# Optimization experiments

Measured on AMD Instinct MI355X. Metric: run time of the kernel, lower is better.

Reference implementation:

```python
import jax, jax.numpy as jnp
import numpy as np

B, HI, WI, CV, CT, T = 8, 64, 64, 512, 512, 77
HH, DH = 8, 64
TOP_M, TOPP, CLAMP_LOGIT, TAU, ALPHA0 = 5, 0.9, 2.0, 0.5, 0.1


def setup_inputs() -> dict:
    key = jax.random.key(0)
    ks = jax.random.split(key, 12)
    s = 0.02
    w = lambda k, shp: jax.random.normal(k, shp, jnp.float32) * s
    return {
        "visual": jax.random.normal(ks[0], (B, HI, WI, CV), jnp.float32),
        "text": jax.random.normal(ks[1], (B, T, CT), jnp.float32),
        "ln1_g": jnp.ones((CV,), jnp.float32), "ln1_b": jnp.zeros((CV,), jnp.float32),
        "ln2_g": jnp.ones((CV,), jnp.float32), "ln2_b": jnp.zeros((CV,), jnp.float32),
        "Wq": w(ks[2], (CV, CV)), "bq": jnp.zeros((CV,), jnp.float32),
        "Wk": w(ks[3], (CT, CV)), "bk": jnp.zeros((CV,), jnp.float32),
        "Wv": w(ks[4], (CT, CV)), "bv": jnp.zeros((CV,), jnp.float32),
        "Wo": w(ks[5], (CV, CV)), "bo": jnp.zeros((CV,), jnp.float32),
        "Wg": w(ks[6], (CV, 1)), "bg": jnp.zeros((1,), jnp.float32),
        "W1": w(ks[7], (CV, 4 * CV)), "b1": jnp.zeros((4 * CV,), jnp.float32),
        "W2": w(ks[8], (4 * CV, CV)), "b2": jnp.zeros((CV,), jnp.float32),
        "logit_scale": jnp.asarray(np.log(1.0 / 0.07), jnp.float32),
        "alpha": jnp.asarray(ALPHA0, jnp.float32),
    }


def _ln(x, g, b, eps=1e-5):
    m = x.mean(-1, keepdims=True)
    v = ((x - m) ** 2).mean(-1, keepdims=True)
    return (x - m) * jax.lax.rsqrt(v + eps) * g + b


def _l2norm(t, eps=1e-6):  # F.normalize: x / max(||x||, eps)
    return t / jnp.maximum(jnp.linalg.norm(t, axis=-1, keepdims=True), eps)


def _sam_forward(visual, text, ln1_g, ln1_b, ln2_g, ln2_b, Wq, bq, Wk, bk, Wv, bv,
                 Wo, bo, Wg, bg, W1, b1, W2, b2, logit_scale, alpha):
    Bx, Hi, Wi, C = visual.shape
    N = Hi * Wi
    x = _ln(visual, ln1_g, ln1_b).reshape(Bx, N, C)          # pre-LN, [B,N,Cv]
    q_full = x @ Wq + bq
    k_full = text @ Wk + bk
    v_full = text @ Wv + bv
    pad = jnp.abs(text).sum(-1) <= 1e-6                      # [B,T] all-zero tokens
    q = _l2norm(q_full).reshape(Bx, N, HH, DH)               # normalize over full Cv, then split heads
    k = _l2norm(k_full).reshape(Bx, -1, HH, DH)
    v = v_full.reshape(Bx, -1, HH, DH)
    scale = jnp.exp(jnp.clip(logit_scale, -CLAMP_LOGIT, CLAMP_LOGIT)) / jnp.sqrt(jnp.float32(DH))
    sim = jnp.einsum("bnhd,bthd->bnht", q, k) * scale        # [B,N,H,T]
    sim = jnp.where(pad[:, None, None, :], -jnp.inf, sim)
    # top-m sparsify (keep entries >= kth largest)
    if TOP_M < sim.shape[-1]:
        kth = jax.lax.top_k(sim, TOP_M)[0][..., -1:]
        sim = jnp.where(sim >= kth, sim, -jnp.inf)
    attn = jax.nn.softmax(sim, axis=-1)
    # top-p nucleus: sort desc, keep cum<=p (always keep top-1), scatter back, renorm
    idx = jnp.argsort(-attn, axis=-1)
    prob = jnp.take_along_axis(attn, idx, axis=-1)
    keep = (jnp.cumsum(prob, axis=-1) <= TOPP).astype(attn.dtype)
    keep = keep.at[..., 0].set(1.0)
    inv = jnp.argsort(idx, axis=-1)
    sparse = jnp.take_along_axis(keep * prob, inv, axis=-1)
    attn = sparse / jnp.maximum(sparse.sum(-1, keepdims=True), 1e-6)
    # entropy-based confidence, [B,N,1]
    ah = attn.transpose(0, 2, 1, 3)                          # [B,H,N,T]
    maxp = ah.max(-1, keepdims=True)
    t_eff = jnp.maximum((ah > 0).astype(attn.dtype).sum(-1, keepdims=True), 1.0)
    denom = jnp.log(jnp.maximum(t_eff, 2.0))
    pc = jnp.maximum(ah, 1e-8)
    entropy = -(pc * jnp.log(pc)).sum(-1, keepdims=True) / denom
    conf = jnp.clip(maxp * (1.0 - entropy), 0.0, 1.0).mean(axis=1)
    aligned = jnp.einsum("bnht,bthd->bnhd", attn, v).reshape(Bx, N, C)
    aligned = aligned @ Wo + bo
    # trust region: cap ||aligned|| at tau * rms(x)
    x_rms = jnp.sqrt((x ** 2).mean(-1, keepdims=True)) + 1e-6
    a_norm = jnp.sqrt((aligned ** 2).sum(-1, keepdims=True))
    aligned = aligned * jnp.minimum(TAU * x_rms / jnp.maximum(a_norm, 1e-6), 1.0)
    gate = jax.nn.sigmoid(x @ Wg + bg) * conf
    y = x + alpha * gate * aligned
    h = jax.nn.gelu(_ln(y, ln2_g, ln2_b) @ W1 + b1, approximate=False)
    y = y + (h @ W2 + b2)
    return y.reshape(Bx, Hi, Wi, C)


def reference(visual, text, ln1_g, ln1_b, ln2_g, ln2_b, Wq, bq, Wk, bk, Wv, bv,
              Wo, bo, Wg, bg, W1, b1, W2, b2, logit_scale, alpha):
    return _sam_forward(visual, text, ln1_g, ln1_b, ln2_g, ln2_b, Wq, bq, Wk, bk,
                        Wv, bv, Wo, bo, Wg, bg, W1, b1, W2, b2, logit_scale, alpha)
```

## Files before the change

### kernel.cpp

```cpp
#include <hip/hip_runtime.h>
#include <hip/hip_bf16.h>
#include <math.h>

#define NROW 32768
#define CVC  512
#define T77  77
#define BT   616
#define HHC  8
#define DHC  64

typedef __attribute__((ext_vector_type(8))) short bf16x8;
typedef __attribute__((ext_vector_type(4))) float f32x4;

__device__ __forceinline__ void gload_lds16(const void* g, void* l) {
  __builtin_amdgcn_global_load_lds(
      (__attribute__((address_space(1))) void*)g,
      (__attribute__((address_space(3))) void*)l, 16, 0, 0);
}

__device__ __forceinline__ float wave_reduce_sum(float v) {
  #pragma unroll
  for (int s = 32; s > 0; s >>= 1) v += __shfl_xor(v, s, 64);
  return v;
}

__global__ __launch_bounds__(256)
void stats1_kernel(const float* __restrict__ visual, const float* __restrict__ g,
                   const float* __restrict__ b, const float* __restrict__ Wg,
                   const float* __restrict__ bg,
                   float* __restrict__ mean1, float* __restrict__ rstd1,
                   float* __restrict__ xrms, float* __restrict__ gpre,
                   __hip_bfloat16* __restrict__ xbf) {
  const int lane = threadIdx.x & 63;
  const int row  = blockIdx.x * 4 + (threadIdx.x >> 6);
  const float* vr = visual + (size_t)row * CVC + lane * 8;
  float4 va = *(const float4*)vr;
  float4 vb = *(const float4*)(vr + 4);
  float v[8] = {va.x, va.y, va.z, va.w, vb.x, vb.y, vb.z, vb.w};
  float s = 0.f;
  #pragma unroll
  for (int i = 0; i < 8; i++) s += v[i];
  float m = wave_reduce_sum(s) * (1.0f / CVC);
  float s2 = 0.f;
  #pragma unroll
  for (int i = 0; i < 8; i++) { float d = v[i] - m; s2 += d * d; }
  float rs = rsqrtf(wave_reduce_sum(s2) * (1.0f / CVC) + 1e-5f);
  const float4 g0 = *(const float4*)(g + lane * 8), g1v = *(const float4*)(g + lane * 8 + 4);
  const float4 b0 = *(const float4*)(b + lane * 8), b1v = *(const float4*)(b + lane * 8 + 4);
  const float4 w0 = *(const float4*)(Wg + lane * 8), w1 = *(const float4*)(Wg + lane * 8 + 4);
  float gg[8] = {g0.x, g0.y, g0.z, g0.w, g1v.x, g1v.y, g1v.z, g1v.w};
  float bb[8] = {b0.x, b0.y, b0.z, b0.w, b1v.x, b1v.y, b1v.z, b1v.w};
  float ww[8] = {w0.x, w0.y, w0.z, w0.w, w1.x, w1.y, w1.z, w1.w};
  float x[8], sx2 = 0.f, sg = 0.f;
  union { bf16x8 v8; __hip_bfloat16 h[8]; } u;
  #pragma unroll
  for (int i = 0; i < 8; i++) {
    x[i] = (v[i] - m) * rs * gg[i] + bb[i];
    sx2 += x[i] * x[i];
    sg  += x[i] * ww[i];
    u.h[i] = __float2bfloat16(x[i]);
  }
  *(bf16x8*)(xbf + (size_t)row * CVC + lane * 8) = u.v8;
  sx2 = wave_reduce_sum(sx2);
  sg  = wave_reduce_sum(sg);
  if (lane == 0) {
    mean1[row] = m; rstd1[row] = rs;
    xrms[row] = sqrtf(sx2 * (1.0f / CVC)) + 1e-6f;
    gpre[row] = sg + bg[0];
  }
}

__global__ void convT_kernel(const float* __restrict__ W, __hip_bfloat16* __restrict__ Wt,
                             int K, int N) {
  __shared__ float t[32][33];
  int n0 = blockIdx.x * 32, k0 = blockIdx.y * 32;
  int tx = threadIdx.x, ty = threadIdx.y;
  #pragma unroll
  for (int i = 0; i < 32; i += 8) t[ty + i][tx] = W[(size_t)(k0 + ty + i) * N + n0 + tx];
  __syncthreads();
  #pragma unroll
  for (int i = 0; i < 32; i += 8)
    Wt[(size_t)(n0 + ty + i) * K + k0 + tx] = __float2bfloat16(t[tx][ty + i]);
}

template<int EPI>
__global__ __launch_bounds__(512, 2)
void mfma_gemm(const __hip_bfloat16* __restrict__ A, const __hip_bfloat16* __restrict__ Bt,
               const float* __restrict__ bias, float* __restrict__ out,
               __hip_bfloat16* __restrict__ outbf, float* __restrict__ ps,
               int M, int N, int K) {
  __shared__ __align__(16) char lds[131072];
  const int tid = threadIdx.x;
  const int lane = tid & 63;
  const int wid  = tid >> 6;

  const int nwg  = gridDim.x * gridDim.y;
  const int orig = blockIdx.y * gridDim.x + blockIdx.x;
  const int wg   = (orig & 7) * (nwg >> 3) + (orig >> 3);
  const int bx = wg % gridDim.x;
  const int by = wg / gridDim.x;
  const int bm = by * 256, bn = bx * 256;

  const int wm = wid >> 2, wn = wid & 3;
  const int lrow = lane & 15, kq = lane >> 4;

  f32x4 acc[8][4] = {};

  const int r_in = lane >> 3;
  const int cblk = (lane & 7) ^ r_in;
  const __hip_bfloat16* gA = A  + (size_t)(bm + r_in) * K + cblk * 8;
  const __hip_bfloat16* gB = Bt + (size_t)(bn + r_in) * K + cblk * 8;
  char* ldsA = lds;
  char* ldsB = lds + 65536;

  auto stageA = [&](int buf, int k0, int half) {
    #pragma unroll
    for (int j = 0; j < 2; j++) {
      int R0 = half * 128 + wid * 16 + j * 8;
      gload_lds16(gA + (size_t)R0 * K + k0, ldsA + buf * 32768 + R0 * 128);
    }
  };
  auto stageB = [&](int buf, int k0, int half) {
    #pragma unroll
    for (int j = 0; j < 2; j++) {
      int R0 = half * 128 + wid * 16 + j * 8;
      gload_lds16(gB + (size_t)R0 * K + k0, ldsB + buf * 32768 + R0 * 128);
    }
  };

  const int swz = lrow & 7;
  auto ldA = [&](int buf, int m, int kk) -> bf16x8 {
    int r = wm * 128 + m * 16 + lrow;
    int blk = (kk * 4 + kq) ^ swz;
    return *(const bf16x8*)(ldsA + buf * 32768 + r * 128 + blk * 16);
  };
  auto ldB = [&](int buf, int n, int kk) -> bf16x8 {
    int r = wn * 64 + n * 16 + lrow;
    int blk = (kk * 4 + kq) ^ swz;
    return *(const bf16x8*)(ldsB + buf * 32768 + r * 128 + blk * 16);
  };

  const int NT = K >> 6;
  stageB(0, 0, 0); stageB(0, 0, 1);
  stageA(0, 0, 0); stageA(0, 0, 1);
  stageB(1, 64, 0); stageB(1, 64, 1);

  bf16x8 af[4][2], bfv[4][2];
  for (int t = 0; t < NT; ++t) {
    const int cur = t & 1;
    if (t < NT - 1) {
      asm volatile("s_waitcnt vmcnt(4)" ::: "memory");
    } else {
      asm volatile("s_waitcnt vmcnt(0)" ::: "memory");
    }
    __builtin_amdgcn_s_barrier();
    asm volatile("" ::: "memory");

    #pragma unroll
    for (int m = 0; m < 4; m++) { af[m][0] = ldA(cur, m, 0); af[m][1] = ldA(cur, m, 1); }
    #pragma unroll
    for (int n = 0; n < 2; n++) { bfv[n][0] = ldB(cur, n, 0); bfv[n][1] = ldB(cur, n, 1); }
    if (t + 1 < NT) stageA(cur ^ 1, (t + 1) << 6, 0);
    __builtin_amdgcn_s_setprio(1);
    #pragma unroll
    for (int m = 0; m < 4; m++)
      #pragma unroll
      for (int n = 0; n < 2; n++) {
        acc[m][n] = __builtin_amdgcn_mfma_f32_16x16x32_bf16(af[m][0], bfv[n][0], acc[m][n], 0, 0, 0);
        acc[m][n] = __builtin_amdgcn_mfma_f32_16x16x32_bf16(af[m][1], bfv[n][1], acc[m][n], 0, 0, 0);
      }
    __builtin_amdgcn_s_setprio(0);

    #pragma unroll
    for (int n = 2; n < 4; n++) { bfv[n][0] = ldB(cur, n, 0); bfv[n][1] = ldB(cur, n, 1); }
    if (t + 1 < NT) stageA(cur ^ 1, (t + 1) << 6, 1);
    __builtin_amdgcn_s_setprio(1);
    #pragma unroll
    for (int m = 0; m < 4; m++)
      #pragma unroll
      for (int n = 2; n < 4; n++) {
        acc[m][n] = __builtin_amdgcn_mfma_f32_16x16x32_bf16(af[m][0], bfv[n][0], acc[m][n], 0, 0, 0);
        acc[m][n] = __builtin_amdgcn_mfma_f32_16x16x32_bf16(af[m][1], bfv[n][1], acc[m][n], 0, 0, 0);
      }
    __builtin_amdgcn_s_setprio(0);

    asm volatile("s_waitcnt lgkmcnt(0)" ::: "memory");
    __builtin_amdgcn_s_barrier();
    asm volatile("" ::: "memory");

    #pragma unroll
    for (int m = 0; m < 4; m++) { af[m][0] = ldA(cur, m + 4, 0); af[m][1] = ldA(cur, m + 4, 1); }
    if (t + 2 < NT) stageB(cur, (t + 2) << 6, 0);
    __builtin_amdgcn_s_setprio(1);
    #pragma unroll
    for (int m = 0; m < 4; m++)
      #pragma unroll
      for (int n = 0; n < 2; n++) {
        acc[m + 4][n] = __builtin_amdgcn_mfma_f32_16x16x32_bf16(af[m][0], bfv[n][0], acc[m + 4][n], 0, 0, 0);
        acc[m + 4][n] = __builtin_amdgcn_mfma_f32_16x16x32_bf16(af[m][1], bfv[n][1], acc[m + 4][n], 0, 0, 0);
      }
    __builtin_amdgcn_s_setprio(0);

    if (t + 2 < NT) stageB(cur, (t + 2) << 6, 1);
    __builtin_amdgcn_s_setprio(1);
    #pragma unroll
    for (int m = 0; m < 4; m++)
      #pragma unroll
      for (int n = 2; n < 4; n++) {
        acc[m + 4][n] = __builtin_amdgcn_mfma_f32_16x16x32_bf16(af[m][0], bfv[n][0], acc[m + 4][n], 0, 0, 0);
        acc[m + 4][n] = __builtin_amdgcn_mfma_f32_16x16x32_bf16(af[m][1], bfv[n][1], acc[m + 4][n], 0, 0, 0);
      }
    __builtin_amdgcn_s_setprio(0);
  }

  const int c0 = bn + wn * 64 + lrow;
  if (EPI == 1) {
    __syncthreads();
    char* eb = lds + wid * 16384;
    #pragma unroll
    for (int n = 0; n < 4; n++) {
      float bval = bias[c0 + n * 16];
      #pragma unroll
      for (int m = 0; m < 8; m++) {
        #pragma unroll
        for (int rg = 0; rg < 4; rg++) {
          int lr  = m * 16 + kq * 4 + rg;
          int lcb = (n * 32 + lrow * 2) ^ (kq << 5);
          float v = acc[m][n][rg] + bval;
          float ge = v / (1.0f + __expf(v * (-1.5957691216f - 0.0713548162f * v * v)));
          *(__hip_bfloat16*)(eb + lr * 128 + lcb) = __float2bfloat16(ge);
        }
      }
    }
    asm volatile("s_waitcnt lgkmcnt(0)" ::: "memory");
    __builtin_amdgcn_sched_barrier(0);
    const int rr = lane >> 3, bb = lane & 7;
    #pragma unroll
    for (int it = 0; it < 16; it++) {
      int lr  = it * 8 + rr;
      int lcb = (bb << 4) ^ (((lr >> 2) & 3) << 5);
      uint4 v = *(const uint4*)(eb + lr * 128 + lcb);
      size_t go = (size_t)(bm + wm * 128 + lr) * N + (bn + wn * 64 + bb * 8);
      *(uint4*)(&outbf[go]) = v;
    }
  } else if (EPI == 3) {
    __syncthreads();
    char* eb = lds + wid * 16384;
    float bv4[4];
    #pragma unroll
    for (int n = 0; n < 4; n++) bv4[n] = bias[c0 + n * 16];
    const int psi = (bn >> 8) * 4 + wn;
    #pragma unroll
    for (int m = 0; m < 8; m++) {
      #pragma unroll
      for (int rg = 0; rg < 4; rg++) {
        int lr = m * 16 + kq * 4 + rg;
        float ss = 0.f;
        #pragma unroll
        for (int n = 0; n < 4; n++) {
          float v = acc[m][n][rg] + bv4[n];
          ss += v * v;
          int lcb = (n * 32 + lrow * 2) ^ (kq << 5);
          *(__hip_bfloat16*)(eb + lr * 128 + lcb) = __float2bfloat16(v);
        }
        ss += __shfl_xor(ss, 1, 64); ss += __shfl_xor(ss, 2, 64);
        ss += __shfl_xor(ss, 4, 64); ss += __shfl_xor(ss, 8, 64);
        if (lrow == 0) ps[(size_t)psi * M + (bm + wm * 128 + lr)] = ss;
      }
    }
    asm volatile("s_waitcnt lgkmcnt(0)" ::: "memory");
    __builtin_amdgcn_sched_barrier(0);
    const int rr = lane >> 3, bb = lane & 7;
    #pragma unroll
    for (int it = 0; it < 16; it++) {
      int lr  = it * 8 + rr;
      int lcb = (bb << 4) ^ (((lr >> 2) & 3) << 5);
      uint4 v = *(const uint4*)(eb + lr * 128 + lcb);
      size_t go = (size_t)(bm + wm * 128 + lr) * N + (bn + wn * 64 + bb * 8);
      *(uint4*)(&outbf[go]) = v;
    }
  } else {
    __syncthreads();
    char* eb = lds + wid * 16384;
    const int rr = lane >> 4, bb = lane & 15;
    #pragma unroll
    for (int half = 0; half < 2; half++) {
      if (half) {
        asm volatile("s_waitcnt lgkmcnt(0)" ::: "memory");
        __builtin_amdgcn_sched_barrier(0);
      }
      #pragma unroll
      for (int n = 0; n < 4; n++) {
        float bval = bias[c0 + n * 16];
        #pragma unroll
        for (int m = 0; m < 4; m++) {
          #pragma unroll
          for (int rg = 0; rg < 4; rg++) {
            int lr  = m * 16 + kq * 4 + rg;
            int byo = (n * 64 + lrow * 4) ^ (kq << 6);
            *(float*)(eb + lr * 256 + byo) = acc[half * 4 + m][n][rg] + bval;
          }
        }
      }
      asm volatile("s_waitcnt lgkmcnt(0)" ::: "memory");
      __builtin_amdgcn_sched_barrier(0);
      #pragma unroll
      for (int it = 0; it < 16; it++) {
        int lr  = it * 4 + rr;
        int byo = (bb * 16) ^ (((lr >> 2) & 3) << 6);
        float4 v4 = *(const float4*)(eb + lr * 256 + byo);
        size_t go = (size_t)(bm + wm * 128 + half * 64 + lr) * N + (bn + wn * 64 + bb * 4);
        if (EPI == 0) {
          *(float4*)(&out[go]) = v4;
        } else {
          const float4 o = *(const float4*)(&out[go]);
          v4.x += o.x; v4.y += o.y; v4.z += o.z; v4.w += o.w;
          *(float4*)(&out[go]) = v4;
        }
      }
    }
  }
}

__global__ void kv2_gemm(const float* __restrict__ A,
                         const float* __restrict__ Wk, const float* __restrict__ bk,
                         const float* __restrict__ Wv, const float* __restrict__ bv,
                         float* __restrict__ KF, float* __restrict__ VF,
                         int M, int K, int N) {
  __shared__ float As[16][68];
  __shared__ float Bs[16][68];
  const bool isV = blockIdx.y >= 10;
  const float* W    = isV ? Wv : Wk;
  const float* bias = isV ? bv : bk;
  float* out        = isV ? VF : KF;
  int tid = threadIdx.x;
  int bm = (isV ? blockIdx.y - 10 : blockIdx.y) * 64, bn = blockIdx.x * 64;
  int ty = tid >> 4, tx = tid & 15;
  float acc[4][4] = {};
  for (int k0 = 0; k0 < K; k0 += 16) {
    #pragma unroll
    for (int i = 0; i < 4; i++) {
      int idx = tid + i * 256;
      int mm = idx >> 4, kk = idx & 15;
      int row = bm + mm;
      As[kk][mm] = (row < M) ? A[(size_t)row * K + k0 + kk] : 0.f;
    }
    #pragma unroll
    for (int i = 0; i < 4; i++) {
      int idx = tid + i * 256;
      int kk = idx >> 6, nn = idx & 63;
      Bs[kk][nn] = W[(size_t)(k0 + kk) * N + bn + nn];
    }
    __syncthreads();
    #pragma unroll
    for (int kk = 0; kk < 16; kk++) {
      float4 av = *(const float4*)&As[kk][ty * 4];
      float4 bv4 = *(const float4*)&Bs[kk][tx * 4];
      float a_[4] = {av.x, av.y, av.z, av.w};
      float b_[4] = {bv4.x, bv4.y, bv4.z, bv4.w};
      #pragma unroll
      for (int i = 0; i < 4; i++)
        #pragma unroll
        for (int j = 0; j < 4; j++)
          acc[i][j] = fmaf(a_[i], b_[j], acc[i][j]);
    }
    __syncthreads();
  }
  #pragma unroll
  for (int i = 0; i < 4; i++) {
    int row = bm + ty * 4 + i;
    if (row >= M) continue;
    #pragma unroll
    for (int j = 0; j < 4; j++) {
      int col = bn + tx * 4 + j;
      out[(size_t)row * N + col] = acc[i][j] + bias[col];
    }
  }
}

__global__ __launch_bounds__(256)
void l2norm_kernel(const __hip_bfloat16* __restrict__ qf, const float* __restrict__ ps,
                   __hip_bfloat16* __restrict__ qbf) {
  const int lane = threadIdx.x & 63;
  const int row  = blockIdx.x * 4 + (threadIdx.x >> 6);
  float s = 0.f;
  #pragma unroll
  for (int j = 0; j < 8; j++) s += ps[(size_t)j * NROW + row];
  float inv = 1.0f / fmaxf(sqrtf(s), 1e-6f);
  union { bf16x8 v8; __hip_bfloat16 h[8]; } u;
  u.v8 = *(const bf16x8*)(qf + (size_t)row * CVC + lane * 8);
  #pragma unroll
  for (int i = 0; i < 8; i++)
    u.h[i] = __float2bfloat16(__bfloat162float(u.h[i]) * inv);
  *(bf16x8*)(qbf + (size_t)row * CVC + lane * 8) = u.v8;
}

__global__ __launch_bounds__(256)
void knorm_kernel(float* __restrict__ kf, const float* __restrict__ text,
                  int* __restrict__ pad) {
  const int lane = threadIdx.x & 63;
  const int row  = blockIdx.x * 4 + (threadIdx.x >> 6);
  float* p = kf + (size_t)row * CVC + lane * 8;
  const float* tx = text + (size_t)row * CVC + lane * 8;
  float4 va = *(const float4*)p;
  float4 vb = *(const float4*)(p + 4);
  float4 ta = *(const float4*)tx;
  float4 tb = *(const float4*)(tx + 4);
  float v[8] = {va.x, va.y, va.z, va.w, vb.x, vb.y, vb.z, vb.w};
  float t[8] = {ta.x, ta.y, ta.z, ta.w, tb.x, tb.y, tb.z, tb.w};
  float s = 0.f, a = 0.f;
  #pragma unroll
  for (int i = 0; i < 8; i++) { s += v[i] * v[i]; a += fabsf(t[i]); }
  s = wave_reduce_sum(s);
  a = wave_reduce_sum(a);
  float inv = 1.0f / fmaxf(sqrtf(s), 1e-6f);
  float4 o0 = {v[0] * inv, v[1] * inv, v[2] * inv, v[3] * inv};
  float4 o1 = {v[4] * inv, v[5] * inv, v[6] * inv, v[7] * inv};
  *(float4*)p = o0;
  *(float4*)(p + 4) = o1;
  if (lane == 0) pad[row] = (a <= 1e-6f) ? 1 : 0;
}

__global__ void kbf_kernel(const float* __restrict__ kf, __hip_bfloat16* __restrict__ kbf) {
  int bh = blockIdx.x;
  int b = bh >> 3, h = bh & 7;
  int tid = threadIdx.x;
  for (int i = tid; i < 80 * 64; i += 256) {
    int t = i >> 6, d = i & 63;
    float v = (t < T77) ? kf[(size_t)(b * T77 + t) * CVC + h * DHC + d] : 0.0f;
    kbf[(size_t)bh * (80 * 64) + i] = __float2bfloat16(v);
  }
}

__global__ __launch_bounds__(256)
void simA_kernel(const __hip_bfloat16* __restrict__ qbf, const __hip_bfloat16* __restrict__ kbf,
                 float* __restrict__ sim) {
  const int tid = threadIdx.x;
  const int wid = tid >> 6, lane = tid & 63;
  const int r0 = blockIdx.x * 64 + wid * 16;
  const int b = (blockIdx.x * 64) >> 12;
  const int lrow = lane & 15, kq = lane >> 4;
  const __hip_bfloat16* qrow = qbf + (size_t)(r0 + lrow) * CVC;
  for (int h = 0; h < HHC; h++) {
    const __hip_bfloat16* kb = kbf + (size_t)(b * 8 + h) * (80 * 64);
    f32x4 acc[5] = {};
    #pragma unroll
    for (int ks = 0; ks < 2; ks++) {
      bf16x8 af = *(const bf16x8*)(qrow + h * DHC + ks * 32 + kq * 8);
      #pragma unroll
      for (int n = 0; n < 5; n++) {
        bf16x8 bf = *(const bf16x8*)(kb + (size_t)(n * 16 + lrow) * DHC + ks * 32 + kq * 8);
        acc[n] = __builtin_amdgcn_mfma_f32_16x16x32_bf16(af, bf, acc[n], 0, 0, 0);
      }
    }
    #pragma unroll
    for (int n = 0; n < 5; n++)
      #pragma unroll
      for (int rg = 0; rg < 4; rg++)
        sim[(size_t)(r0 + kq * 4 + rg) * 640 + h * 80 + n * 16 + lrow] = acc[n][rg];
  }
}

__global__ __launch_bounds__(256)
void attnB_kernel(const float* __restrict__ sim, const float* __restrict__ vf,
                  const int* __restrict__ pad, const float* __restrict__ ls,
                  float* __restrict__ conf_out, __hip_bfloat16* __restrict__ abf) {
  __shared__ float spr[32][HHC][5];
  __shared__ int   sti[32][HHC][5];
  __shared__ float sconf[256];
  __shared__ float sbias[80];
  const int tid = threadIdx.x;
  const int r = tid >> 3, h = tid & 7;
  const int r0 = blockIdx.x * 32;
  const int b = r0 >> 12;
  const float lsv = fminf(fmaxf(ls[0], -2.0f), 2.0f);
  const float scale = expf(lsv) * 0.125f;

  if (tid < 80) sbias[tid] = (tid < T77 && !pad[b * T77 + tid]) ? 0.0f : -INFINITY;
  __syncthreads();

  float t0 = -INFINITY, t1 = -INFINITY, t2 = -INFINITY, t3 = -INFINITY, t4 = -INFINITY;
  int   i0 = -1, i1 = -1, i2 = -1, i3 = -1, i4 = -1;
  const float4* simp = (const float4*)(sim + (size_t)(r0 + r) * 640 + h * 80);
  #pragma unroll
  for (int tt = 0; tt < 20; tt++) {
    float4 v4 = simp[tt];
    #pragma unroll
    for (int j = 0; j < 4; j++) {
      int t = tt * 4 + j;
      float sv = (j == 0 ? v4.x : j == 1 ? v4.y : j == 2 ? v4.z : v4.w);
      float s = sv * scale + sbias[t];
      if (s > t4) {
        t4 = s; i4 = t;
        if (t4 > t3) { float f = t3; t3 = t4; t4 = f; int x = i3; i3 = i4; i4 = x; }
        if (t3 > t2) { float f = t2; t2 = t3; t3 = f; int x = i2; i2 = i3; i3 = x; }
        if (t2 > t1) { float f = t1; t1 = t2; t2 = f; int x = i1; i1 = i2; i2 = x; }
        if (t1 > t0) { float f = t0; t0 = t1; t1 = f; int x = i0; i0 = i1; i1 = x; }
      }
    }
  }

  float e0 = (t0 == -INFINITY) ? 0.f : expf(t0 - t0);
  float e1 = (t1 == -INFINITY) ? 0.f : expf(t1 - t0);
  float e2 = (t2 == -INFINITY) ? 0.f : expf(t2 - t0);
  float e3 = (t3 == -INFINITY) ? 0.f : expf(t3 - t0);
  float e4 = (t4 == -INFINITY) ? 0.f : expf(t4 - t0);
  float invs = 1.0f / (e0 + e1 + e2 + e3 + e4);
  float p0 = e0 * invs, p1 = e1 * invs, p2 = e2 * invs, p3 = e3 * invs, p4 = e4 * invs;
  float c1 = p0 + p1, c2 = c1 + p2, c3 = c2 + p3, c4 = c3 + p4;
  bool k1 = (c1 <= 0.9f), k2 = (c2 <= 0.9f), k3 = (c3 <= 0.9f), k4 = (c4 <= 0.9f);
  float skeep = p0 + (k1 ? p1 : 0.f) + (k2 ? p2 : 0.f) + (k3 ? p3 : 0.f) + (k4 ? p4 : 0.f);
  float rn = 1.0f / fmaxf(skeep, 1e-6f);
  float w0 = p0 * rn, w1 = k1 ? p1 * rn : 0.f, w2 = k2 ? p2 * rn : 0.f,
        w3 = k3 ? p3 * rn : 0.f, w4 = k4 ? p4 * rn : 0.f;
  int nnz = (w0 > 0.f) + (w1 > 0.f) + (w2 > 0.f) + (w3 > 0.f) + (w4 > 0.f);
  float ent = 0.f;
  {
    float pc;
    pc = fmaxf(w0, 1e-8f); ent -= pc * logf(pc);
    pc = fmaxf(w1, 1e-8f); ent -= pc * logf(pc);
    pc = fmaxf(w2, 1e-8f); ent -= pc * logf(pc);
    pc = fmaxf(w3, 1e-8f); ent -= pc * logf(pc);
    pc = fmaxf(w4, 1e-8f); ent -= pc * logf(pc);
  }
  ent += (float)(T77 - 5) * 1.8420681e-7f;
  float denom = logf(fmaxf(fmaxf((float)nnz, 1.0f), 2.0f));
  ent /= denom;
  float confh = fminf(fmaxf(w0 * (1.0f - ent), 0.f), 1.f);

  spr[r][h][0] = w0; spr[r][h][1] = w1; spr[r][h][2] = w2; spr[r][h][3] = w3; spr[r][h][4] = w4;
  sti[r][h][0] = i0; sti[r][h][1] = i1; sti[r][h][2] = i2; sti[r][h][3] = i3; sti[r][h][4] = i4;
  sconf[tid] = confh;
  __syncthreads();

  if (tid < 32) {
    float s = 0.f;
    #pragma unroll
    for (int j = 0; j < 8; j++) s += sconf[tid * 8 + j];
    conf_out[r0 + tid] = s * 0.125f;
  }

  #pragma unroll
  for (int it = 0; it < 64; it++) {
    int idx = tid + it * 256;
    int rr = idx >> 9, c = idx & 511, hh = c >> 6;
    float a = 0.f;
    #pragma unroll
    for (int i = 0; i < 5; i++) {
      float pr = spr[rr][hh][i]; int t = sti[rr][hh][i];
      if (pr > 0.f && t >= 0) a = fmaf(pr, vf[((size_t)(b * T77 + t)) * CVC + c], a);
    }
    abf[(size_t)(r0 + rr) * CVC + c] = __float2bfloat16(a);
  }
}

__global__ __launch_bounds__(256)
void combine_kernel(const __hip_bfloat16* __restrict__ alnbf, const float* __restrict__ ps,
                    const float* __restrict__ visual,
                    const float* __restrict__ m1, const float* __restrict__ r1,
                    const float* __restrict__ g1, const float* __restrict__ b1v,
                    const float* __restrict__ xrms, const float* __restrict__ gpre,
                    const float* __restrict__ conf, const float* __restrict__ alpha,
                    const float* __restrict__ g2, const float* __restrict__ b2v,
                    float* __restrict__ dout, __hip_bfloat16* __restrict__ ybf) {
  const int lane = threadIdx.x & 63;
  const int row  = blockIdx.x * 4 + (threadIdx.x >> 6);
  float s2 = 0.f;
  #pragma unroll
  for (int j = 0; j < 8; j++) s2 += ps[(size_t)j * NROW + row];
  float an = sqrtf(s2);
  float factor = fminf(0.5f * xrms[row] / fmaxf(an, 1e-6f), 1.0f);
  float gate = conf[row] / (1.0f + expf(-gpre[row]));
  float coef = alpha[0] * gate * factor;
  float mm = m1[row], rs = r1[row];
  union { bf16x8 v8; __hip_bfloat16 h[8]; } ua;
  ua.v8 = *(const bf16x8*)(alnbf + (size_t)row * CVC + lane * 8);
  float av[8];
  #pragma unroll
  for (int i = 0; i < 8; i++) av[i] = __bfloat162float(ua.h[i]);
  const float* vr = visual + (size_t)row * CVC + lane * 8;
  float4 va = *(const float4*)vr;
  float4 vb = *(const float4*)(vr + 4);
  float v[8] = {va.x, va.y, va.z, va.w, vb.x, vb.y, vb.z, vb.w};
  const float4 ga = *(const float4*)(g1 + lane * 8), gb = *(const float4*)(g1 + lane * 8 + 4);
  const float4 ba = *(const float4*)(b1v + lane * 8), bb2 = *(const float4*)(b1v + lane * 8 + 4);
  float gg[8] = {ga.x, ga.y, ga.z, ga.w, gb.x, gb.y, gb.z, gb.w};
  float bbv[8] = {ba.x, ba.y, ba.z, ba.w, bb2.x, bb2.y, bb2.z, bb2.w};
  float y[8], sy = 0.f;
  #pragma unroll
  for (int i = 0; i < 8; i++) {
    float x = (v[i] - mm) * rs * gg[i] + bbv[i];
    y[i] = x + coef * av[i];
    sy += y[i];
  }
  float* orow = dout + (size_t)row * CVC + lane * 8;
  float4 o0 = {y[0], y[1], y[2], y[3]};
  float4 o1 = {y[4], y[5], y[6], y[7]};
  *(float4*)orow = o0;
  *(float4*)(orow + 4) = o1;
  float ym = wave_reduce_sum(sy) * (1.0f / CVC);
  float var = 0.f;
  #pragma unroll
  for (int i = 0; i < 8; i++) { float d = y[i] - ym; var += d * d; }
  var = wave_reduce_sum(var) * (1.0f / CVC);
  float rs2 = rsqrtf(var + 1e-5f);
  const float4 g2a = *(const float4*)(g2 + lane * 8), g2b = *(const float4*)(g2 + lane * 8 + 4);
  const float4 b2a = *(const float4*)(b2v + lane * 8), b2b = *(const float4*)(b2v + lane * 8 + 4);
  float g2v[8] = {g2a.x, g2a.y, g2a.z, g2a.w, g2b.x, g2b.y, g2b.z, g2b.w};
  float b2vv[8] = {b2a.x, b2a.y, b2a.z, b2a.w, b2b.x, b2b.y, b2b.z, b2b.w};
  union { bf16x8 v8; __hip_bfloat16 h[8]; } u;
  #pragma unroll
  for (int i = 0; i < 8; i++)
    u.h[i] = __float2bfloat16((y[i] - ym) * rs2 * g2v[i] + b2vv[i]);
  *(bf16x8*)(ybf + (size_t)row * CVC + lane * 8) = u.v8;
}

extern "C" void kernel_launch(void* const* d_in, const int* in_sizes, int n_in,
                              void* d_out, int out_size, void* d_ws, size_t ws_size,
                              hipStream_t stream) {
  const float* visual = (const float*)d_in[0];
  const float* text   = (const float*)d_in[1];
  const float* ln1_g  = (const float*)d_in[2];
  const float* ln1_b  = (const float*)d_in[3];
  const float* ln2_g  = (const float*)d_in[4];
  const float* ln2_b  = (const float*)d_in[5];
  const float* Wq = (const float*)d_in[6];  const float* bq = (const float*)d_in[7];
  const float* Wk = (const float*)d_in[8];  const float* bk = (const float*)d_in[9];
  const float* Wv = (const float*)d_in[10]; const float* bv = (const float*)d_in[11];
  const float* Wo = (const float*)d_in[12]; const float* bo = (const float*)d_in[13];
  const float* Wg = (const float*)d_in[14]; const float* bg = (const float*)d_in[15];
  const float* W1 = (const float*)d_in[16]; const float* b1 = (const float*)d_in[17];
  const float* W2 = (const float*)d_in[18]; const float* b2 = (const float*)d_in[19];
  const float* ls    = (const float*)d_in[20];
  const float* alpha = (const float*)d_in[21];
  float* out = (float*)d_out;

  char* base = (char*)d_ws;
  __hip_bfloat16* H     = (__hip_bfloat16*)base;
  __hip_bfloat16* QBF2  = (__hip_bfloat16*)base;
  __hip_bfloat16* ALNBF = (__hip_bfloat16*)base;
  float* SIM  = (float*)base;
  __hip_bfloat16* CBF = (__hip_bfloat16*)(base + ((size_t)128 << 20));
  char* p = base + ((size_t)160 << 20);
  __hip_bfloat16* WqT = (__hip_bfloat16*)p; p += (size_t)512 * 512 * 2;
  __hip_bfloat16* WoT = (__hip_bfloat16*)p; p += (size_t)512 * 512 * 2;
  __hip_bfloat16* W1T = (__hip_bfloat16*)p; p += (size_t)2048 * 512 * 2;
  __hip_bfloat16* W2T = (__hip_bfloat16*)p; p += (size_t)512 * 2048 * 2;
  float* KF = (float*)p; p += (size_t)BT * CVC * 4;
  float* VF = (float*)p; p += (size_t)BT * CVC * 4;
  int* PADF = (int*)p;  p += 4096;
  float* MEAN1 = (float*)p; p += (size_t)NROW * 4;
  float* RSTD1 = (float*)p; p += (size_t)NROW * 4;
  float* XRMS  = (float*)p; p += (size_t)NROW * 4;
  float* GPRE  = (float*)p; p += (size_t)NROW * 4;
  float* CONF  = (float*)p; p += (size_t)NROW * 4;
  __hip_bfloat16* KBF = (__hip_bfloat16*)p; p += (size_t)64 * 80 * 64 * 2;
  float* PS = (float*)p; p += (size_t)8 * NROW * 4;

  stats1_kernel<<<NROW / 4, 256, 0, stream>>>(visual, ln1_g, ln1_b, Wg, bg,
                                              MEAN1, RSTD1, XRMS, GPRE, CBF);
  convT_kernel<<<dim3(16, 16), dim3(32, 8), 0, stream>>>(Wq, WqT, 512, 512);
  convT_kernel<<<dim3(16, 16), dim3(32, 8), 0, stream>>>(Wo, WoT, 512, 512);
  convT_kernel<<<dim3(64, 16), dim3(32, 8), 0, stream>>>(W1, W1T, 512, 2048);
  convT_kernel<<<dim3(16, 64), dim3(32, 8), 0, stream>>>(W2, W2T, 2048, 512);

  mfma_gemm<3><<<dim3(2, 128), 512, 0, stream>>>(CBF, WqT, bq, nullptr, QBF2, PS,
                                                 NROW, 512, 512);
  l2norm_kernel<<<NROW / 4, 256, 0, stream>>>(QBF2, PS, CBF);

  kv2_gemm<<<dim3(8, 20), 256, 0, stream>>>(text, Wk, bk, Wv, bv, KF, VF, BT, CVC, CVC);
  knorm_kernel<<<BT / 4, 256, 0, stream>>>(KF, text, PADF);
  kbf_kernel<<<64, 256, 0, stream>>>(KF, KBF);

  simA_kernel<<<NROW / 64, 256, 0, stream>>>(CBF, KBF, SIM);
  attnB_kernel<<<NROW / 32, 256, 0, stream>>>(SIM, VF, PADF, ls, CONF, CBF);

  mfma_gemm<3><<<dim3(2, 128), 512, 0, stream>>>(CBF, WoT, bo, nullptr, ALNBF, PS,
                                                 NROW, 512, 512);

  combine_kernel<<<NROW / 4, 256, 0, stream>>>(ALNBF, PS, visual, MEAN1, RSTD1, ln1_g, ln1_b,
                                               XRMS, GPRE, CONF, alpha, ln2_g, ln2_b, out, CBF);

  mfma_gemm<1><<<dim3(8, 128), 512, 0, stream>>>(CBF, W1T, b1, nullptr, H, nullptr,
                                                 NROW, 2048, 512);

  mfma_gemm<2><<<dim3(2, 128), 512, 0, stream>>>(H, W2T, b2, out, nullptr, nullptr,
                                                 NROW, 512, 2048);
}
```

Before: 520.9 us.

## Fold Q normalization into attention scale and merge small prep kernels

Removes the separate q l2norm pass and instead applies the per-row inverse norm as a scale on the similarity scores inside the attention kernel, so the unnormalized bf16 Q feeds simA directly. The K normalize and K bf16 repack kernels are merged into one kernel that writes the head-split bf16 layout directly, and the four weight-transpose launches become one. This saves a full 32Kx512 bf16 read/write pass plus several launches. SIM is moved to a separate workspace offset so it no longer aliases QBF2. A small rounding difference is possible because Q is no longer normalized before the bf16 dot product.

```diff
diff --git a/kernel.cpp b/kernel.cpp
--- a/kernel.cpp
+++ b/kernel.cpp
@@ -70,11 +70,19 @@
   }
 }
 
-__global__ void convT_kernel(const float* __restrict__ W, __hip_bfloat16* __restrict__ Wt,
-                             int K, int N) {
+__global__ void convT_all(const float* __restrict__ Wq_, const float* __restrict__ Wo_,
+                          const float* __restrict__ W1_, const float* __restrict__ W2_,
+                          __hip_bfloat16* __restrict__ WqT, __hip_bfloat16* __restrict__ WoT,
+                          __hip_bfloat16* __restrict__ W1T, __hip_bfloat16* __restrict__ W2T) {
   __shared__ float t[32][33];
-  int n0 = blockIdx.x * 32, k0 = blockIdx.y * 32;
-  int tx = threadIdx.x, ty = threadIdx.y;
+  const int id = blockIdx.x;
+  const float* W; __hip_bfloat16* Wt; int K, N, bx, by;
+  if (id < 256)       { W = Wq_; Wt = WqT; K = 512;  N = 512;  int l = id;        bx = l & 15; by = l >> 4; }
+  else if (id < 512)  { W = Wo_; Wt = WoT; K = 512;  N = 512;  int l = id - 256;  bx = l & 15; by = l >> 4; }
+  else if (id < 1536) { W = W1_; Wt = W1T; K = 512;  N = 2048; int l = id - 512;  bx = l & 63; by = l >> 6; }
+  else                { W = W2_; Wt = W2T; K = 2048; N = 512;  int l = id - 1536; bx = l & 15; by = l >> 4; }
+  const int n0 = bx * 32, k0 = by * 32;
+  const int tx = threadIdx.x, ty = threadIdx.y;
   #pragma unroll
   for (int i = 0; i < 32; i += 8) t[ty + i][tx] = W[(size_t)(k0 + ty + i) * N + n0 + tx];
   __syncthreads();
@@ -379,28 +387,17 @@
 }
 
 __global__ __launch_bounds__(256)
-void l2norm_kernel(const __hip_bfloat16* __restrict__ qf, const float* __restrict__ ps,
-                   __hip_bfloat16* __restrict__ qbf) {
+void kprep_kernel(const float* __restrict__ kf, const float* __restrict__ text,
+                  __hip_bfloat16* __restrict__ kbf, int* __restrict__ pad) {
   const int lane = threadIdx.x & 63;
   const int row  = blockIdx.x * 4 + (threadIdx.x >> 6);
-  float s = 0.f;
-  #pragma unroll
-  for (int j = 0; j < 8; j++) s += ps[(size_t)j * NROW + row];
-  float inv = 1.0f / fmaxf(sqrtf(s), 1e-6f);
-  union { bf16x8 v8; __hip_bfloat16 h[8]; } u;
-  u.v8 = *(const bf16x8*)(qf + (size_t)row * CVC + lane * 8);
-  #pragma unroll
-  for (int i = 0; i < 8; i++)
-    u.h[i] = __float2bfloat16(__bfloat162float(u.h[i]) * inv);
-  *(bf16x8*)(qbf + (size_t)row * CVC + lane * 8) = u.v8;
-}
-
-__global__ __launch_bounds__(256)
-void knorm_kernel(float* __restrict__ kf, const float* __restrict__ text,
-                  int* __restrict__ pad) {
-  const int lane = threadIdx.x & 63;
-  const int row  = blockIdx.x * 4 + (threadIdx.x >> 6);
-  float* p = kf + (size_t)row * CVC + lane * 8;
+  if (blockIdx.x == 0) {
+    for (int i = threadIdx.x; i < 64 * 3 * 64; i += 256) {
+      int bh = i / 192, rem = i % 192, tt = 77 + rem / 64, d = rem & 63;
+      kbf[(size_t)bh * (80 * 64) + tt * 64 + d] = __float2bfloat16(0.f);
+    }
+  }
+  const float* p  = kf + (size_t)row * CVC + lane * 8;
   const float* tx = text + (size_t)row * CVC + lane * 8;
   float4 va = *(const float4*)p;
   float4 vb = *(const float4*)(p + 4);
@@ -414,22 +411,13 @@
   s = wave_reduce_sum(s);
   a = wave_reduce_sum(a);
   float inv = 1.0f / fmaxf(sqrtf(s), 1e-6f);
-  float4 o0 = {v[0] * inv, v[1] * inv, v[2] * inv, v[3] * inv};
-  float4 o1 = {v[4] * inv, v[5] * inv, v[6] * inv, v[7] * inv};
-  *(float4*)p = o0;
-  *(float4*)(p + 4) = o1;
+  const int b = row / T77, tt = row - b * T77;
+  const int h = lane >> 3, d0 = (lane & 7) * 8;
+  union { bf16x8 v8; __hip_bfloat16 h8[8]; } u;
+  #pragma unroll
+  for (int i = 0; i < 8; i++) u.h8[i] = __float2bfloat16(v[i] * inv);
+  *(bf16x8*)(kbf + ((size_t)(b * 8 + h) * 80 + tt) * 64 + d0) = u.v8;
   if (lane == 0) pad[row] = (a <= 1e-6f) ? 1 : 0;
-}
-
-__global__ void kbf_kernel(const float* __restrict__ kf, __hip_bfloat16* __restrict__ kbf) {
-  int bh = blockIdx.x;
-  int b = bh >> 3, h = bh & 7;
-  int tid = threadIdx.x;
-  for (int i = tid; i < 80 * 64; i += 256) {
-    int t = i >> 6, d = i & 63;
-    float v = (t < T77) ? kf[(size_t)(b * T77 + t) * CVC + h * DHC + d] : 0.0f;
-    kbf[(size_t)bh * (80 * 64) + i] = __float2bfloat16(v);
-  }
 }
 
 __global__ __launch_bounds__(256)
@@ -464,11 +452,13 @@
 __global__ __launch_bounds__(256)
 void attnB_kernel(const float* __restrict__ sim, const float* __restrict__ vf,
                   const int* __restrict__ pad, const float* __restrict__ ls,
+                  const float* __restrict__ psq,
                   float* __restrict__ conf_out, __hip_bfloat16* __restrict__ abf) {
   __shared__ float spr[32][HHC][5];
   __shared__ int   sti[32][HHC][5];
   __shared__ float sconf[256];
   __shared__ float sbias[80];
+  __shared__ float sinvq[32];
   const int tid = threadIdx.x;
   const int r = tid >> 3, h = tid & 7;
   const int r0 = blockIdx.x * 32;
@@ -477,8 +467,15 @@
   const float scale = expf(lsv) * 0.125f;
 
   if (tid < 80) sbias[tid] = (tid < T77 && !pad[b * T77 + tid]) ? 0.0f : -INFINITY;
+  if (tid < 32) {
+    float s2 = 0.f;
+    #pragma unroll
+    for (int j = 0; j < 8; j++) s2 += psq[(size_t)j * NROW + r0 + tid];
+    sinvq[tid] = 1.0f / fmaxf(sqrtf(s2), 1e-6f);
+  }
   __syncthreads();
 
+  const float srow = scale * sinvq[r];
   float t0 = -INFINITY, t1 = -INFINITY, t2 = -INFINITY, t3 = -INFINITY, t4 = -INFINITY;
   int   i0 = -1, i1 = -1, i2 = -1, i3 = -1, i4 = -1;
   const float4* simp = (const float4*)(sim + (size_t)(r0 + r) * 640 + h * 80);
@@ -489,7 +486,7 @@
     for (int j = 0; j < 4; j++) {
       int t = tt * 4 + j;
       float sv = (j == 0 ? v4.x : j == 1 ? v4.y : j == 2 ? v4.z : v4.w);
-      float s = sv * scale + sbias[t];
+      float s = sv * srow + sbias[t];
       if (s > t4) {
         t4 = s; i4 = t;
         if (t4 > t3) { float f = t3; t3 = t4; t4 = f; int x = i3; i3 = i4; i4 = x; }
@@ -636,10 +633,10 @@
   float* out = (float*)d_out;
 
   char* base = (char*)d_ws;
-  __hip_bfloat16* H     = (__hip_bfloat16*)base;
   __hip_bfloat16* QBF2  = (__hip_bfloat16*)base;
   __hip_bfloat16* ALNBF = (__hip_bfloat16*)base;
-  float* SIM  = (float*)base;
+  __hip_bfloat16* H     = (__hip_bfloat16*)base;
+  float* SIM  = (float*)(base + ((size_t)32 << 20));
   __hip_bfloat16* CBF = (__hip_bfloat16*)(base + ((size_t)128 << 20));
   char* p = base + ((size_t)160 << 20);
   __hip_bfloat16* WqT = (__hip_bfloat16*)p; p += (size_t)512 * 512 * 2;
@@ -659,21 +656,16 @@
 
   stats1_kernel<<<NROW / 4, 256, 0, stream>>>(visual, ln1_g, ln1_b, Wg, bg,
                                               MEAN1, RSTD1, XRMS, GPRE, CBF);
-  convT_kernel<<<dim3(16, 16), dim3(32, 8), 0, stream>>>(Wq, WqT, 512, 512);
-  convT_kernel<<<dim3(16, 16), dim3(32, 8), 0, stream>>>(Wo, WoT, 512, 512);
-  convT_kernel<<<dim3(64, 16), dim3(32, 8), 0, stream>>>(W1, W1T, 512, 2048);
-  convT_kernel<<<dim3(16, 64), dim3(32, 8), 0, stream>>>(W2, W2T, 2048, 512);
+  convT_all<<<2560, dim3(32, 8), 0, stream>>>(Wq, Wo, W1, W2, WqT, WoT, W1T, W2T);
 
   mfma_gemm<3><<<dim3(2, 128), 512, 0, stream>>>(CBF, WqT, bq, nullptr, QBF2, PS,
                                                  NROW, 512, 512);
-  l2norm_kernel<<<NROW / 4, 256, 0, stream>>>(QBF2, PS, CBF);
 
   kv2_gemm<<<dim3(8, 20), 256, 0, stream>>>(text, Wk, bk, Wv, bv, KF, VF, BT, CVC, CVC);
-  knorm_kernel<<<BT / 4, 256, 0, stream>>>(KF, text, PADF);
-  kbf_kernel<<<64, 256, 0, stream>>>(KF, KBF);
-
-  simA_kernel<<<NROW / 64, 256, 0, stream>>>(CBF, KBF, SIM);
-  attnB_kernel<<<NROW / 32, 256, 0, stream>>>(SIM, VF, PADF, ls, CONF, CBF);
+  kprep_kernel<<<BT / 4, 256, 0, stream>>>(KF, text, KBF, PADF);
+
+  simA_kernel<<<NROW / 64, 256, 0, stream>>>(QBF2, KBF, SIM);
+  attnB_kernel<<<NROW / 32, 256, 0, stream>>>(SIM, VF, PADF, ls, PS, CONF, CBF);
 
   mfma_gemm<3><<<dim3(2, 128), 512, 0, stream>>>(CBF, WoT, bo, nullptr, ALNBF, PS,
                                                  NROW, 512, 512);
```

Result: faster. 503.0 us, median of 2 (-3.4%).
